# Optimization experiments

Measured on AMD Instinct MI355X. Metric: run time of the kernel, lower is better.

## Reference

```python
import jax, jax.numpy as jnp
import numpy as np

B, L, DIM = 2, 2048, 2048
N_HEADS, N_KV_HEADS = 32, 8
HEAD_DIM = DIM // N_HEADS  # 64
SCALE = HEAD_DIM ** -0.5


def setup_inputs() -> dict:
    key = jax.random.key(0)
    ks = jax.random.split(key, 6)
    s = 0.02
    x = jax.random.normal(ks[0], (B, L, DIM), dtype=jnp.float32)
    wq = jax.random.normal(ks[1], (N_HEADS * HEAD_DIM, DIM), dtype=jnp.float32) * s
    wk = jax.random.normal(ks[2], (N_KV_HEADS * HEAD_DIM, DIM), dtype=jnp.float32) * s
    wv = jax.random.normal(ks[3], (N_KV_HEADS * HEAD_DIM, DIM), dtype=jnp.float32) * s
    wo = jax.random.normal(ks[4], (DIM, N_HEADS * HEAD_DIM), dtype=jnp.float32) * s
    # standard RoPE frequencies: theta = 10000^(-2i/d), angle = pos * theta
    inv_freq = 1.0 / (10000.0 ** (jnp.arange(0, HEAD_DIM, 2, dtype=jnp.float32) / HEAD_DIM))
    angles = jnp.arange(L, dtype=jnp.float32)[:, None] * inv_freq[None, :]  # [L, HEAD_DIM//2]
    freqs_cos = jnp.cos(angles)
    freqs_sin = jnp.sin(angles)
    # additive causal mask [1, 1, L, L]
    causal = jnp.tril(jnp.ones((L, L), dtype=bool))
    mask = jnp.where(causal, 0.0, -1e9).astype(jnp.float32)[None, None]
    return {"x": x, "wq": wq, "wk": wk, "wv": wv, "wo": wo,
            "freqs_cos": freqs_cos, "freqs_sin": freqs_sin, "mask": mask}


def _apply_rope(t, cos, sin):
    # t: [B, H, L, D]; complex pairing is (even, odd) interleaved along D
    te, to = t[..., 0::2], t[..., 1::2]
    cos = cos[None, None, : t.shape[2], :]
    sin = sin[None, None, : t.shape[2], :]
    re = te * cos - to * sin
    im = te * sin + to * cos
    return jnp.stack([re, im], axis=-1).reshape(t.shape)


def reference(x, wq, wk, wv, wo, freqs_cos, freqs_sin, mask):
    b, l, _ = x.shape
    q = (x @ wq.T).reshape(b, l, N_HEADS, HEAD_DIM).transpose(0, 2, 1, 3)
    k = (x @ wk.T).reshape(b, l, N_KV_HEADS, HEAD_DIM).transpose(0, 2, 1, 3)
    v = (x @ wv.T).reshape(b, l, N_KV_HEADS, HEAD_DIM).transpose(0, 2, 1, 3)
    q = _apply_rope(q, freqs_cos, freqs_sin)
    k = _apply_rope(k, freqs_cos, freqs_sin)
    repeats = N_HEADS // N_KV_HEADS
    k = jnp.repeat(k, repeats, axis=1)
    v = jnp.repeat(v, repeats, axis=1)
    scores = jnp.einsum("bhqd,bhkd->bhqk", q, k) * SCALE + mask
    probs = jax.nn.softmax(scores, axis=-1)
    out = jnp.einsum("bhqk,bhkd->bhqd", probs, v)
    out = out.transpose(0, 2, 1, 3).reshape(b, l, N_HEADS * HEAD_DIM)
    return out @ wo.T
```

## Files before the change

kernel.cpp:

```cpp
#include <hip/hip_runtime.h>
#include <hip/hip_bf16.h>
#include <stdint.h>

typedef __attribute__((ext_vector_type(8))) short bf16x8;
typedef __attribute__((ext_vector_type(4))) float f32x4;
typedef __attribute__((ext_vector_type(16))) float f32x16;
typedef __attribute__((ext_vector_type(4))) unsigned int u32x4;

#define B_    2
#define L_    2048
#define DIM_  2048
#define NH_   32
#define NKV_  8
#define HD_   64
#define KVD_  512
#define CLOG_ 0.1803368801111244f

__device__ __forceinline__ unsigned short f2bf(float f) {
  unsigned u = __float_as_uint(f);
  u += 0x7fff + ((u >> 16) & 1);
  return (unsigned short)(u >> 16);
}
__device__ __forceinline__ unsigned cvtpk(float lo, float hi_) {
  unsigned r;
  asm("v_cvt_pk_bf16_f32 %0, %1, %2" : "=v"(r) : "v"(lo), "v"(hi_));
  return r;
}
__device__ __forceinline__ float bf2f(unsigned short h) {
  return __uint_as_float(((unsigned)h) << 16);
}
__device__ __forceinline__ void plswap2(unsigned &a, unsigned &b, int hi) {
#if __has_builtin(__builtin_amdgcn_permlane32_swap)
  auto r = __builtin_amdgcn_permlane32_swap(a, b, false, false);
  a = (unsigned)r[0]; b = (unsigned)r[1];
#else
  unsigned xa = (unsigned)__shfl_xor((int)a, 32);
  unsigned xb = (unsigned)__shfl_xor((int)b, 32);
  unsigned na = hi ? xb : a, nb = hi ? b : xa;
  a = na; b = nb;
#endif
}

#define GLDS16(gsrc, ldst) __builtin_amdgcn_global_load_lds( \
    (const __attribute__((address_space(1))) unsigned int*)(gsrc), \
    (__attribute__((address_space(3))) unsigned int*)(ldst), 16, 0, 0)

__global__ void cvt_all(const float* __restrict__ x,  const float* __restrict__ wq,
                        const float* __restrict__ wk, const float* __restrict__ wv,
                        const float* __restrict__ wo,
                        unsigned short* __restrict__ xb,  unsigned short* __restrict__ wqb,
                        unsigned short* __restrict__ wkb, unsigned short* __restrict__ wvb,
                        unsigned short* __restrict__ wob) {
  int i = blockIdx.x * blockDim.x + threadIdx.x;
  const float* src; unsigned short* dst; int off;
  if (i < 2097152)      { src = x;  dst = xb;  off = i; }
  else if (i < 3145728) { src = wq; dst = wqb; off = i - 2097152; }
  else if (i < 3407872) { src = wk; dst = wkb; off = i - 3145728; }
  else if (i < 3670016) { src = wv; dst = wvb; off = i - 3407872; }
  else                  { src = wo; dst = wob; off = i - 3670016; }
  float4 v = reinterpret_cast<const float4*>(src)[off];
  ushort4 o;
  o.x = f2bf(v.x); o.y = f2bf(v.y); o.z = f2bf(v.z); o.w = f2bf(v.w);
  reinterpret_cast<ushort4*>(dst)[off] = o;
}

template<int OUTMODE>
__device__ __forceinline__ void gemm128_core(
    const unsigned short* __restrict__ A,
    const unsigned short* __restrict__ W,
    void* __restrict__ C, int N, int K, int m0, int n0,
    unsigned short (*As)[128 * 64], unsigned short (*Bs)[128 * 64])
{
  const int tid = threadIdx.x;
  const int lane = tid & 63, wid = tid >> 6;
  const int wm = wid >> 1, wn = wid & 1;
  const int r = lane & 15, g = lane >> 4;
  const int rsw = (r & 7) << 4;
  f32x4 acc[4][4] = {};

  auto STAGE = [&](int buf, int k0) {
#pragma unroll
    for (int p = 0; p < 4; ++p) {
      int off = (p * 256 + tid) * 16;
      int row = off >> 7;
      int colb = (off & 127) ^ ((row & 7) << 4);
      GLDS16((const char*)A + ((size_t)(m0 + row) * K + k0) * 2 + colb,
             (char*)As[buf] + off);
      GLDS16((const char*)W + ((size_t)(n0 + row) * K + k0) * 2 + colb,
             (char*)Bs[buf] + off);
    }
  };

  const int nt = K >> 6;
  STAGE(0, 0);
  asm volatile("s_waitcnt vmcnt(0)" ::: "memory");
  __builtin_amdgcn_s_barrier();
  int cur = 0;
  for (int kt = 0; kt < nt; ++kt) {
    if (kt + 1 < nt) {
      STAGE(cur ^ 1, (kt + 1) << 6);
      asm volatile("s_waitcnt vmcnt(8)" ::: "memory");
    } else {
      asm volatile("s_waitcnt vmcnt(0)" ::: "memory");
    }
    __builtin_amdgcn_s_barrier();
    __builtin_amdgcn_sched_barrier(0);
    const char* Ab = (const char*)As[cur];
    const char* Bb = (const char*)Bs[cur];
    __builtin_amdgcn_s_setprio(1);
#pragma unroll
    for (int kk = 0; kk < 2; ++kk) {
      bf16x8 af[4], bfv[4];
#pragma unroll
      for (int i = 0; i < 4; ++i)
        af[i] = *reinterpret_cast<const bf16x8*>(
            Ab + (wm * 64 + i * 16 + r) * 128 + ((kk * 64 + g * 16) ^ rsw));
#pragma unroll
      for (int i = 0; i < 4; ++i)
        bfv[i] = *reinterpret_cast<const bf16x8*>(
            Bb + (wn * 64 + i * 16 + r) * 128 + ((kk * 64 + g * 16) ^ rsw));
#pragma unroll
      for (int i = 0; i < 4; ++i)
#pragma unroll
        for (int j = 0; j < 4; ++j)
          acc[i][j] = __builtin_amdgcn_mfma_f32_16x16x32_bf16(af[i], bfv[j], acc[i][j], 0, 0, 0);
    }
    __builtin_amdgcn_s_setprio(0);
    asm volatile("s_waitcnt lgkmcnt(0)" ::: "memory");
    __builtin_amdgcn_s_barrier();
    cur ^= 1;
  }

  if (OUTMODE == 2) {
#pragma unroll
    for (int i = 0; i < 4; ++i)
#pragma unroll
      for (int jf = 0; jf < 4; ++jf) {
        int col = n0 + wn * 64 + jf * 16 + r;
        int kvi = col >> 6, d = col & 63;
        int tok = m0 + wm * 64 + i * 16 + g * 4;
        int bb = tok >> 11, tl = tok & (L_ - 1);
        uint2 u;
        u.x = cvtpk(acc[i][jf][0], acc[i][jf][1]);
        u.y = cvtpk(acc[i][jf][2], acc[i][jf][3]);
        *reinterpret_cast<uint2*>((unsigned short*)C +
            ((size_t)((bb * NKV_ + kvi) * HD_ + d)) * L_ + tl) = u;
      }
  } else {
#pragma unroll
    for (int i = 0; i < 4; ++i)
#pragma unroll
      for (int jf = 0; jf < 4; ++jf)
#pragma unroll
        for (int j = 0; j < 4; ++j) {
          size_t row = (size_t)(m0 + wm * 64 + i * 16 + g * 4 + j);
          size_t col = (size_t)(n0 + wn * 64 + jf * 16 + r);
          float v = acc[i][jf][j];
          if (OUTMODE == 1) ((float*)C)[row * N + col] = v;
          else ((unsigned short*)C)[row * N + col] = f2bf(v);
        }
  }
}

template<int OUT_F32>
__global__ __launch_bounds__(256) void gemm_bt(
    const unsigned short* __restrict__ A,
    const unsigned short* __restrict__ W,
    void* __restrict__ C, int M, int N, int K)
{
  __shared__ unsigned short As[2][128 * 64];
  __shared__ unsigned short Bs[2][128 * 64];
  gemm128_core<OUT_F32 ? 1 : 0>(A, W, C, N, K, blockIdx.y * 128, blockIdx.x * 128, As, Bs);
}

__global__ __launch_bounds__(256) void gemm_qkv(
    const unsigned short* __restrict__ A,
    const unsigned short* __restrict__ Wq,
    const unsigned short* __restrict__ Wk,
    const unsigned short* __restrict__ Wv,
    unsigned short* __restrict__ Cq,
    unsigned short* __restrict__ Ck,
    unsigned short* __restrict__ Vt)
{
  __shared__ unsigned short As[2][128 * 64];
  __shared__ unsigned short Bs[2][128 * 64];
  const int bx = blockIdx.x;
  const int m0 = blockIdx.y * 128;
  if (bx < 16)
    gemm128_core<0>(A, Wq, Cq, 2048, DIM_, m0, bx * 128, As, Bs);
  else if (bx < 20)
    gemm128_core<0>(A, Wk, Ck, 512, DIM_, m0, (bx - 16) * 128, As, Bs);
  else
    gemm128_core<2>(A, Wv, Vt, 512, DIM_, m0, (bx - 20) * 128, As, Bs);
}

__global__ void rope_v8(unsigned short* __restrict__ t,
                        const float* __restrict__ fc,
                        const float* __restrict__ fs,
                        int rowElems, int lshift, float scale) {
  int idx = blockIdx.x * blockDim.x + threadIdx.x;
  int row = idx >> lshift;
  if (row >= B_ * L_) return;
  int pos = (idx & ((1 << lshift) - 1)) << 3;
  int l = row & (L_ - 1);
  int i0 = (pos & 63) >> 1;
  unsigned short* p = t + (size_t)row * rowElems + pos;
  uint4 v = *reinterpret_cast<const uint4*>(p);
  float4 c4 = *reinterpret_cast<const float4*>(fc + l * 32 + i0);
  float4 s4 = *reinterpret_cast<const float4*>(fs + l * 32 + i0);
  float cc[4] = {c4.x * scale, c4.y * scale, c4.z * scale, c4.w * scale};
  float ss[4] = {s4.x * scale, s4.y * scale, s4.z * scale, s4.w * scale};
  unsigned wds[4] = {v.x, v.y, v.z, v.w};
  uint4 o;
  unsigned ow[4];
#pragma unroll
  for (int k = 0; k < 4; ++k) {
    float te = bf2f((unsigned short)(wds[k] & 0xffff));
    float to = bf2f((unsigned short)(wds[k] >> 16));
    ow[k] = cvtpk(te * cc[k] - to * ss[k], te * ss[k] + to * cc[k]);
  }
  o.x = ow[0]; o.y = ow[1]; o.z = ow[2]; o.w = ow[3];
  *reinterpret_cast<uint4*>(p) = o;
}

__global__ __launch_bounds__(512, 4) void attn_kernel(
    const unsigned short* __restrict__ Q,
    const unsigned short* __restrict__ K,
    const unsigned short* __restrict__ Vt,
    const float* __restrict__ fc, const float* __restrict__ fs,
    unsigned short* __restrict__ AO)
{
  __shared__ unsigned short Ks[2][64 * 64];
  __shared__ unsigned short Vs[2][64 * 64];
  const int tid = threadIdx.x;
  const int lane = tid & 63, w = tid >> 6;
  const int ql = lane & 31, hi = lane >> 5;
  const int id = blockIdx.x;
  const int pairIdx = id >> 1;
  const int bh = pairIdx & 63;
  const int g = pairIdx >> 6;
  const int c = (id & 1) ? (7 - g) : g;
  const int b = bh >> 5, h = bh & 31, kv = h >> 2;
  const int qw = c * 256 + w * 32;
  const int nkt = (c + 1) * 4;

  bf16x8 qf[4];
  {
    const unsigned short* qrow = Q + ((size_t)(b * L_ + qw + ql)) * DIM_ + h * HD_;
    const float* fcr = fc + (size_t)(qw + ql) * 32;
    const float* fsr = fs + (size_t)(qw + ql) * 32;
#pragma unroll
    for (int dk = 0; dk < 4; ++dk) {
      uint4 v = *reinterpret_cast<const uint4*>(qrow + dk * 16 + hi * 8);
      float4 c4 = *reinterpret_cast<const float4*>(fcr + dk * 8 + hi * 4);
      float4 s4 = *reinterpret_cast<const float4*>(fsr + dk * 8 + hi * 4);
      float cc[4] = {c4.x, c4.y, c4.z, c4.w};
      float ss[4] = {s4.x, s4.y, s4.z, s4.w};
      unsigned wd[4] = {v.x, v.y, v.z, v.w};
      u32x4 o;
#pragma unroll
      for (int k2 = 0; k2 < 4; ++k2) {
        float te = bf2f((unsigned short)(wd[k2] & 0xffff));
        float to = bf2f((unsigned short)(wd[k2] >> 16));
        o[k2] = cvtpk((te * cc[k2] - to * ss[k2]) * CLOG_,
                      (te * ss[k2] + to * cc[k2]) * CLOG_);
      }
      qf[dk] = __builtin_bit_cast(bf16x8, o);
    }
  }

  const unsigned short* Kg = K + (size_t)b * L_ * KVD_ + kv * HD_;
  const unsigned short* Vg = Vt + ((size_t)(b * NKV_ + kv)) * HD_ * L_;

  f32x16 oacc0 = {}, oacc1 = {};
  float lrow = 0.f;
  const int rsw = (ql & 7) << 4;

  auto STAGE = [&](int buf, int t) {
    const int k0 = t * 64;
    int off = tid * 16;
    int row = off >> 7;
    int colb = (off & 127) ^ ((row & 7) << 4);
    GLDS16((const char*)Kg + ((size_t)(k0 + row)) * (KVD_ * 2) + colb,
           (char*)Ks[buf] + off);
    GLDS16((const char*)Vg + ((size_t)row) * (L_ * 2) + (size_t)k0 * 2 + colb,
           (char*)Vs[buf] + off);
  };

  int cur = 0;
  STAGE(0, 0);
  asm volatile("s_waitcnt vmcnt(0)" ::: "memory");
  __builtin_amdgcn_s_barrier();

  for (int t = 0; t < nkt; ++t) {
    if (t + 1 < nkt) {
      STAGE(cur ^ 1, t + 1);
      asm volatile("s_waitcnt vmcnt(2)" ::: "memory");
    } else {
      asm volatile("s_waitcnt vmcnt(0)" ::: "memory");
    }
    __builtin_amdgcn_s_barrier();
    __builtin_amdgcn_sched_barrier(0);
    const int k0 = t * 64;
    if (k0 < qw + 32) {
      const char* Kl = (const char*)Ks[cur];
      const char* Vl = (const char*)Vs[cur];
      f32x16 s0 = {}, s1 = {};
      __builtin_amdgcn_s_setprio(1);
#pragma unroll
      for (int dk = 0; dk < 4; ++dk) {
        bf16x8 kf0 = *reinterpret_cast<const bf16x8*>(Kl + ql * 128 + ((dk * 32 + hi * 16) ^ rsw));
        bf16x8 kf1 = *reinterpret_cast<const bf16x8*>(Kl + (32 + ql) * 128 + ((dk * 32 + hi * 16) ^ rsw));
        s0 = __builtin_amdgcn_mfma_f32_32x32x16_bf16(kf0, qf[dk], s0, 0, 0, 0);
        s1 = __builtin_amdgcn_mfma_f32_32x32x16_bf16(kf1, qf[dk], s1, 0, 0, 0);
      }
      __builtin_amdgcn_s_setprio(0);
      float p[32];
      float ps = 0.f;
      if (k0 + 63 > qw) {
        int q = qw + ql;
#pragma unroll
        for (int i = 0; i < 32; ++i) {
          float sv = (i < 16) ? s0[i] : s1[i - 16];
          int kk = k0 + (i >> 4) * 32 + (i & 3) + 8 * ((i & 15) >> 2) + 4 * hi;
          float e = exp2f(sv);
          e = (kk > q) ? 0.f : e;
          p[i] = e; ps += e;
        }
      } else {
#pragma unroll
        for (int i = 0; i < 32; ++i) {
          float sv = (i < 16) ? s0[i] : s1[i - 16];
          p[i] = exp2f(sv); ps += p[i];
        }
      }
      lrow += ps;
      bf16x8 pf[4];
#pragma unroll
      for (int s = 0; s < 4; ++s) {
        int bp = ((s >> 1) << 4) + ((s & 1) << 3);
        unsigned w0 = cvtpk(p[bp + 0], p[bp + 1]);
        unsigned w1 = cvtpk(p[bp + 2], p[bp + 3]);
        unsigned w2 = cvtpk(p[bp + 4], p[bp + 5]);
        unsigned w3 = cvtpk(p[bp + 6], p[bp + 7]);
        plswap2(w0, w2, hi);
        plswap2(w1, w3, hi);
        u32x4 fw;
        fw[0] = w0; fw[1] = w1; fw[2] = w2; fw[3] = w3;
        pf[s] = __builtin_bit_cast(bf16x8, fw);
      }
      __builtin_amdgcn_s_setprio(1);
#pragma unroll
      for (int s = 0; s < 4; ++s) {
        bf16x8 v0 = *reinterpret_cast<const bf16x8*>(Vl + ql * 128 + ((s * 32 + hi * 16) ^ rsw));
        bf16x8 v1 = *reinterpret_cast<const bf16x8*>(Vl + (32 + ql) * 128 + ((s * 32 + hi * 16) ^ rsw));
        oacc0 = __builtin_amdgcn_mfma_f32_32x32x16_bf16(v0, pf[s], oacc0, 0, 0, 0);
        oacc1 = __builtin_amdgcn_mfma_f32_32x32x16_bf16(v1, pf[s], oacc1, 0, 0, 0);
      }
      __builtin_amdgcn_s_setprio(0);
    }
    asm volatile("s_waitcnt lgkmcnt(0)" ::: "memory");
    __builtin_amdgcn_s_barrier();
    cur ^= 1;
  }

  unsigned la = __float_as_uint(lrow), lb = __float_as_uint(lrow);
  plswap2(la, lb, hi);
  float ltot = __uint_as_float(la) + __uint_as_float(lb);
  float inv = 1.f / ltot;
  unsigned short* obase = AO + ((size_t)(b * L_ + qw + ql)) * DIM_ + h * HD_;
#pragma unroll
  for (int g4 = 0; g4 < 4; ++g4) {
    uint2 u;
    u.x = cvtpk(oacc0[g4 * 4 + 0] * inv, oacc0[g4 * 4 + 1] * inv);
    u.y = cvtpk(oacc0[g4 * 4 + 2] * inv, oacc0[g4 * 4 + 3] * inv);
    *reinterpret_cast<uint2*>(obase + g4 * 8 + hi * 4) = u;
    uint2 v;
    v.x = cvtpk(oacc1[g4 * 4 + 0] * inv, oacc1[g4 * 4 + 1] * inv);
    v.y = cvtpk(oacc1[g4 * 4 + 2] * inv, oacc1[g4 * 4 + 3] * inv);
    *reinterpret_cast<uint2*>(obase + 32 + g4 * 8 + hi * 4) = v;
  }
}

extern "C" void kernel_launch(void* const* d_in, const int* in_sizes, int n_in,
                              void* d_out, int out_size, void* d_ws, size_t ws_size,
                              hipStream_t stream) {
  const float* x  = (const float*)d_in[0];
  const float* wq = (const float*)d_in[1];
  const float* wk = (const float*)d_in[2];
  const float* wv = (const float*)d_in[3];
  const float* wo = (const float*)d_in[4];
  const float* fc = (const float*)d_in[5];
  const float* fs = (const float*)d_in[6];
  float* out = (float*)d_out;

  unsigned short* ws  = (unsigned short*)d_ws;
  unsigned short* xb  = ws;
  unsigned short* wqb = xb  + 8388608;
  unsigned short* wkb = wqb + 4194304;
  unsigned short* wvb = wkb + 1048576;
  unsigned short* wob = wvb + 1048576;
  unsigned short* Qb  = wob + 4194304;
  unsigned short* Kb  = Qb  + 8388608;
  unsigned short* Vtb = Kb  + 2097152;
  unsigned short* AOb = Vtb + 2097152;

  cvt_all<<<18432, 256, 0, stream>>>(x, wq, wk, wv, wo, xb, wqb, wkb, wvb, wob);

  gemm_qkv<<<dim3(24, 32), 256, 0, stream>>>(xb, wqb, wkb, wvb, Qb, Kb, Vtb);

  rope_v8<<<1024, 256, 0, stream>>>(Kb, fc, fs, 512, 6, 1.0f);

  attn_kernel<<<512, 512, 0, stream>>>(Qb, Kb, Vtb, fc, fs, AOb);

  gemm_bt<1><<<dim3(16, 32), 256, 0, stream>>>(AOb, wob, out, 4096, 2048, 2048);
}
```

Before: 231.3 us.

## Split attention into 128-row query tiles with snake scheduling and single-barrier pipeline

The attention kernel now launches 1024 blocks of 256 threads, each handling a 128-row query tile instead of 256 rows. Tiles are ordered longest-first in a snake pattern across the causal workload to balance load. The K/V staging loop moves the prefetch to after the barrier, which removes one barrier per iteration at the cost of a full vmcnt(0) wait. Smaller blocks give finer scheduling granularity but reload K/V tiles more often across blocks.

```diff
diff --git a/kernel.cpp b/kernel.cpp
--- a/kernel.cpp
+++ b/kernel.cpp
@@ -223,7 +223,7 @@
   *reinterpret_cast<uint4*>(p) = o;
 }
 
-__global__ __launch_bounds__(512, 4) void attn_kernel(
+__global__ __launch_bounds__(256) void attn_kernel(
     const unsigned short* __restrict__ Q,
     const unsigned short* __restrict__ K,
     const unsigned short* __restrict__ Vt,
@@ -234,15 +234,18 @@
   __shared__ unsigned short Vs[2][64 * 64];
   const int tid = threadIdx.x;
   const int lane = tid & 63, w = tid >> 6;
-  const int ql = lane & 31, hi = lane >> 5;
-  const int id = blockIdx.x;
-  const int pairIdx = id >> 1;
-  const int bh = pairIdx & 63;
-  const int g = pairIdx >> 6;
-  const int c = (id & 1) ? (7 - g) : g;
+  const int ql = lane & 31;
+  const int hi = lane >> 5;
+  const int wid = blockIdx.x;
+  const int j = wid >> 6;
+  const int blk = j >> 2, pos = j & 3;
+  const int base = 15 - 4 * blk;
+  const int qt = (blk & 1) ? (base - 3 + pos) : (base - pos);
+  const int bh = wid & 63;
   const int b = bh >> 5, h = bh & 31, kv = h >> 2;
-  const int qw = c * 256 + w * 32;
-  const int nkt = (c + 1) * 4;
+  const int q0 = qt * 128;
+  const int qw = q0 + w * 32;
+  const int nkt = (q0 + 128) >> 6;
 
   bf16x8 qf[4];
   {
@@ -278,29 +281,26 @@
 
   auto STAGE = [&](int buf, int t) {
     const int k0 = t * 64;
-    int off = tid * 16;
-    int row = off >> 7;
-    int colb = (off & 127) ^ ((row & 7) << 4);
-    GLDS16((const char*)Kg + ((size_t)(k0 + row)) * (KVD_ * 2) + colb,
-           (char*)Ks[buf] + off);
-    GLDS16((const char*)Vg + ((size_t)row) * (L_ * 2) + (size_t)k0 * 2 + colb,
-           (char*)Vs[buf] + off);
+#pragma unroll
+    for (int p = 0; p < 2; ++p) {
+      int off = (p * 256 + tid) * 16;
+      int row = off >> 7;
+      int colb = (off & 127) ^ ((row & 7) << 4);
+      GLDS16((const char*)Kg + ((size_t)(k0 + row)) * (KVD_ * 2) + colb,
+             (char*)Ks[buf] + off);
+      GLDS16((const char*)Vg + ((size_t)row) * (L_ * 2) + (size_t)k0 * 2 + colb,
+             (char*)Vs[buf] + off);
+    }
   };
 
   int cur = 0;
   STAGE(0, 0);
-  asm volatile("s_waitcnt vmcnt(0)" ::: "memory");
-  __builtin_amdgcn_s_barrier();
 
   for (int t = 0; t < nkt; ++t) {
-    if (t + 1 < nkt) {
-      STAGE(cur ^ 1, t + 1);
-      asm volatile("s_waitcnt vmcnt(2)" ::: "memory");
-    } else {
-      asm volatile("s_waitcnt vmcnt(0)" ::: "memory");
-    }
+    asm volatile("s_waitcnt vmcnt(0)" ::: "memory");
     __builtin_amdgcn_s_barrier();
     __builtin_amdgcn_sched_barrier(0);
+    if (t + 1 < nkt) STAGE(cur ^ 1, t + 1);
     const int k0 = t * 64;
     if (k0 < qw + 32) {
       const char* Kl = (const char*)Ks[cur];
@@ -360,7 +360,6 @@
       __builtin_amdgcn_s_setprio(0);
     }
     asm volatile("s_waitcnt lgkmcnt(0)" ::: "memory");
-    __builtin_amdgcn_s_barrier();
     cur ^= 1;
   }
 
@@ -411,7 +410,7 @@
 
   rope_v8<<<1024, 256, 0, stream>>>(Kb, fc, fs, 512, 6, 1.0f);
 
-  attn_kernel<<<512, 512, 0, stream>>>(Qb, Kb, Vtb, fc, fs, AOb);
+  attn_kernel<<<1024, 256, 0, stream>>>(Qb, Kb, Vtb, fc, fs, AOb);
 
   gemm_bt<1><<<dim3(16, 32), 256, 0, stream>>>(AOb, wob, out, 4096, 2048, 2048);
 }
```

Measured after the change: 215.8 us. -6.7%, faster.
